# Kernel optimization log

Measured on AMD Instinct MI355X. Metric: run time of the kernel, lower is better.

The kernel has to match this reference:

```python
import jax, jax.numpy as jnp
import numpy as np
from jax import lax

SIZE = 64
N_PHASES = SIZE * (SIZE - 1) // 2  # 2016
LOSS_DB_CM = 0.5
INSERTION_LOSS_DB = LOSS_DB_CM * 0.1          # per-MZI insertion loss (dB)
LOSS_AMP = 10.0 ** (-INSERTION_LOSS_DB / 20.0)  # amplitude transmission per MZI
NONLINEAR_COEFF = 2.6e-20

# Reck triangular mesh ordering: layer i = 1..SIZE-1, MZIs on adjacent modes (j, j+1)
_MODE_IDX = np.array([j for i in range(1, SIZE) for j in range(i)], dtype=np.int32)


def build_mesh_unitary(phases):
    """Sequentially compose 2x2 MZI rotations into a SIZE x SIZE complex matrix.
    Each MZI with phase theta applies T = loss * [[cos, i sin],[i sin, cos]] to
    adjacent modes (m, m+1). U = T_K ... T_1."""
    U0 = jnp.eye(SIZE, dtype=jnp.complex64)

    def step(U, xs):
        theta, m = xs
        c = jnp.cos(theta).astype(jnp.complex64)
        s = (1j * jnp.sin(theta)).astype(jnp.complex64)
        row_a = U[m]
        row_b = U[m + 1]
        new_a = LOSS_AMP * (c * row_a + s * row_b)
        new_b = LOSS_AMP * (s * row_a + c * row_b)
        U = U.at[m].set(new_a).at[m + 1].set(new_b)
        return U, None

    U, _ = lax.scan(step, U0, (phases, jnp.asarray(_MODE_IDX)))
    return U


def setup_inputs() -> dict:
    key = jax.random.key(0)
    k1, k2, k3 = jax.random.split(key, 3)
    B = 262144
    x_real = jax.random.normal(k1, (B, SIZE), dtype=jnp.float32)
    x_imag = jax.random.normal(k2, (B, SIZE), dtype=jnp.float32)
    # nn.initializers.uniform(scale=2*pi) -> U[0, 2*pi)
    phases = jax.random.uniform(k3, (N_PHASES,), dtype=jnp.float32) * (2.0 * np.pi)
    return {"x_real": x_real, "x_imag": x_imag, "phases": phases}


def reference(x_real, x_imag, phases):
    x = (x_real + 1j * x_imag).astype(jnp.complex64)  # [B, SIZE]
    U = build_mesh_unitary(phases)                    # [SIZE, SIZE] complex64
    # vmapped mesh apply == batched matmul with the composed unitary
    out = x @ U.T                                     # [B, SIZE]
    # Kerr nonlinearity (include_nonlinearity=True)
    optical_power = jnp.abs(out) ** 2
    nonlinear_phase = NONLINEAR_COEFF * optical_power * 1000.0
    out = out * jnp.exp(1j * nonlinear_phase.astype(jnp.complex64))
    return out
```

## Files before the change

### kernel.cpp

```cpp
#include <hip/hip_runtime.h>


#define PSIZE 64
#define N_PHASES 2016
#define NLAYER 63
#define LOSS_AMP 0.99426007f
#define NL_COEFF 2.6e-17f

#define UF32_BYTES (2 * PSIZE * PSIZE * 4)
#define WSPLIT_BYTES (4 * PSIZE * PSIZE * 2)
#define WS_NEED (UF32_BYTES + WSPLIT_BYTES)

typedef __attribute__((ext_vector_type(8))) short sh8;
typedef __attribute__((ext_vector_type(4))) float f32x4;

__device__ __align__(16) float g_U_fallback[2 * PSIZE * PSIZE];

__device__ inline unsigned short f32_to_bf16_rn(float f) {
  unsigned int u = __float_as_uint(f);
  u += 0x7fffu + ((u >> 16) & 1u);
  return (unsigned short)(u >> 16);
}
__device__ inline float bf16_to_f32(unsigned short h) {
  return __uint_as_float(((unsigned int)h) << 16);
}

__device__ inline float rdlane(float v, int l) {
  return __int_as_float(__builtin_amdgcn_readlane(__float_as_int(v), l));
}

__device__ inline unsigned pkbf16(float a, float b) {
  unsigned r;
  asm("v_cvt_pk_bf16_f32 %0, %1, %2" : "=v"(r) : "v"(a), "v"(b));
  return r;
}
__device__ inline float lo16f(unsigned u) { return __uint_as_float(u << 16); }
__device__ inline float hi16f(unsigned u) {
  return __uint_as_float(u & 0xFFFF0000u);
}
__device__ inline sh8 mk8(unsigned a, unsigned b, unsigned c, unsigned d) {
  union { unsigned u[4]; sh8 s; } t;
  t.u[0] = a; t.u[1] = b; t.u[2] = c; t.u[3] = d;
  return t.s;
}

__global__ __launch_bounds__(64, 1) void build_kernel(
    const float* __restrict__ phases,
    float* __restrict__ Uf32,
    unsigned short* __restrict__ Wout) {
  const int tid = threadIdx.x;

  float wre[NLAYER], wim[NLAYER];
#pragma unroll
  for (int li = 0; li < NLAYER; ++li) {
    float c = 1.0f, s = 0.0f;
    if (tid <= li) {
      const float th = phases[(li * (li + 1)) / 2 + tid];
      c = LOSS_AMP * cosf(th);
      s = LOSS_AMP * sinf(th);
    }
    wre[li] = c;
    wim[li] = s;
  }

  float ure[PSIZE], uim[PSIZE];
#pragma unroll
  for (int r = 0; r < PSIZE; ++r) {
    ure[r] = (r == tid) ? 1.0f : 0.0f;
    uim[r] = 0.0f;
  }

#pragma unroll
  for (int li = 0; li < NLAYER; ++li) {
#pragma unroll
    for (int m = 0; m <= li; ++m) {
      const float wc = rdlane(wre[li], m);
      const float ws = rdlane(wim[li], m);
      const float are = ure[m], aim = uim[m];
      const float bre = ure[m + 1], bim = uim[m + 1];
      ure[m]     = fmaf(wc, are, -ws * bim);
      uim[m]     = fmaf(wc, aim,  ws * bre);
      ure[m + 1] = fmaf(wc, bre, -ws * aim);
      uim[m + 1] = fmaf(wc, bim,  ws * are);
    }
  }

  float* Udst = (Uf32 != nullptr) ? Uf32 : g_U_fallback;
#pragma unroll
  for (int r = 0; r < PSIZE; ++r)
    ((float2*)Udst)[r * PSIZE + tid] = make_float2(ure[r], uim[r]);

  if (Wout != nullptr) {
    const int slot = tid >> 3, kin = tid & 7;
#pragma unroll
    for (int n = 0; n < PSIZE; ++n) {
      const int base = n * 64 + ((slot ^ (n & 7)) << 3) + kin;
      const unsigned short rh = f32_to_bf16_rn(ure[n]);
      const unsigned short rl = f32_to_bf16_rn(ure[n] - bf16_to_f32(rh));
      const unsigned short ih = f32_to_bf16_rn(uim[n]);
      const unsigned short il = f32_to_bf16_rn(uim[n] - bf16_to_f32(ih));
      Wout[0 * 4096 + base] = rh;
      Wout[1 * 4096 + base] = rl;
      Wout[2 * 4096 + base] = ih;
      Wout[3 * 4096 + base] = il;
    }
  }
}

__global__ __launch_bounds__(256, 2) void apply_mfma(
    const unsigned short* __restrict__ W,
    const float* __restrict__ xr,
    const float* __restrict__ xi,
    float* __restrict__ out_re,
    float* __restrict__ out_im) {
  __shared__ __align__(16) unsigned short sW[4 * PSIZE * PSIZE];
  {
    const float4* src = (const float4*)W;
    float4* dst = (float4*)sW;
    for (int i = threadIdx.x; i < WSPLIT_BYTES / 16; i += 256) dst[i] = src[i];
  }
  __syncthreads();

  const int lane = threadIdx.x & 63;
  const int wave = threadIdx.x >> 6;
  const int lm = lane & 15;
  const int lg = lane >> 4;
  const long row0 = (long)blockIdx.x * 128 + (long)wave * 32;

  f32x4 accRe[2][4], accIm[2][4];
#pragma unroll
  for (int a = 0; a < 2; ++a)
#pragma unroll
    for (int b = 0; b < 4; ++b) {
      accRe[a][b] = f32x4{0.f, 0.f, 0.f, 0.f};
      accIm[a][b] = f32x4{0.f, 0.f, 0.f, 0.f};
    }

#pragma unroll
  for (int ks = 0; ks < 2; ++ks) {
    sh8 arh[2], arl[2], aih[2], ail[2], anh[2], anl[2];
#pragma unroll
    for (int mt = 0; mt < 2; ++mt) {
      const long r = row0 + mt * 16 + lm;
      const float4* pr = (const float4*)(xr + r * PSIZE + ks * 32 + lg * 8);
      const float4* pi = (const float4*)(xi + r * PSIZE + ks * 32 + lg * 8);
      const float4 v0 = pr[0], v1 = pr[1];
      const float4 w0 = pi[0], w1 = pi[1];

      const unsigned rh0 = pkbf16(v0.x, v0.y), rh1 = pkbf16(v0.z, v0.w);
      const unsigned rh2 = pkbf16(v1.x, v1.y), rh3 = pkbf16(v1.z, v1.w);
      const unsigned rl0 = pkbf16(v0.x - lo16f(rh0), v0.y - hi16f(rh0));
      const unsigned rl1 = pkbf16(v0.z - lo16f(rh1), v0.w - hi16f(rh1));
      const unsigned rl2 = pkbf16(v1.x - lo16f(rh2), v1.y - hi16f(rh2));
      const unsigned rl3 = pkbf16(v1.z - lo16f(rh3), v1.w - hi16f(rh3));
      arh[mt] = mk8(rh0, rh1, rh2, rh3);
      arl[mt] = mk8(rl0, rl1, rl2, rl3);

      const unsigned ih0 = pkbf16(w0.x, w0.y), ih1 = pkbf16(w0.z, w0.w);
      const unsigned ih2 = pkbf16(w1.x, w1.y), ih3 = pkbf16(w1.z, w1.w);
      const unsigned il0 = pkbf16(w0.x - lo16f(ih0), w0.y - hi16f(ih0));
      const unsigned il1 = pkbf16(w0.z - lo16f(ih1), w0.w - hi16f(ih1));
      const unsigned il2 = pkbf16(w1.x - lo16f(ih2), w1.y - hi16f(ih2));
      const unsigned il3 = pkbf16(w1.z - lo16f(ih3), w1.w - hi16f(ih3));
      aih[mt] = mk8(ih0, ih1, ih2, ih3);
      ail[mt] = mk8(il0, il1, il2, il3);
      anh[mt] = mk8(ih0 ^ 0x80008000u, ih1 ^ 0x80008000u,
                    ih2 ^ 0x80008000u, ih3 ^ 0x80008000u);
      anl[mt] = mk8(il0 ^ 0x80008000u, il1 ^ 0x80008000u,
                    il2 ^ 0x80008000u, il3 ^ 0x80008000u);
    }

#pragma unroll
    for (int nt = 0; nt < 4; ++nt) {
      const int n = nt * 16 + lm;
      const int sidx = n * 64 + (((ks * 4 + lg) ^ (n & 7)) << 3);
      const sh8 bRh = *(const sh8*)&sW[0 * 4096 + sidx];
      const sh8 bRl = *(const sh8*)&sW[1 * 4096 + sidx];
      const sh8 bIh = *(const sh8*)&sW[2 * 4096 + sidx];
      const sh8 bIl = *(const sh8*)&sW[3 * 4096 + sidx];
#pragma unroll
      for (int mt = 0; mt < 2; ++mt) {
        f32x4 cr = accRe[mt][nt];
        cr = __builtin_amdgcn_mfma_f32_16x16x32_bf16(arh[mt], bRh, cr, 0, 0, 0);
        cr = __builtin_amdgcn_mfma_f32_16x16x32_bf16(arh[mt], bRl, cr, 0, 0, 0);
        cr = __builtin_amdgcn_mfma_f32_16x16x32_bf16(arl[mt], bRh, cr, 0, 0, 0);
        cr = __builtin_amdgcn_mfma_f32_16x16x32_bf16(anh[mt], bIh, cr, 0, 0, 0);
        cr = __builtin_amdgcn_mfma_f32_16x16x32_bf16(anh[mt], bIl, cr, 0, 0, 0);
        cr = __builtin_amdgcn_mfma_f32_16x16x32_bf16(anl[mt], bIh, cr, 0, 0, 0);
        accRe[mt][nt] = cr;
        f32x4 ci = accIm[mt][nt];
        ci = __builtin_amdgcn_mfma_f32_16x16x32_bf16(arh[mt], bIh, ci, 0, 0, 0);
        ci = __builtin_amdgcn_mfma_f32_16x16x32_bf16(arh[mt], bIl, ci, 0, 0, 0);
        ci = __builtin_amdgcn_mfma_f32_16x16x32_bf16(arl[mt], bIh, ci, 0, 0, 0);
        ci = __builtin_amdgcn_mfma_f32_16x16x32_bf16(aih[mt], bRh, ci, 0, 0, 0);
        ci = __builtin_amdgcn_mfma_f32_16x16x32_bf16(aih[mt], bRl, ci, 0, 0, 0);
        ci = __builtin_amdgcn_mfma_f32_16x16x32_bf16(ail[mt], bRh, ci, 0, 0, 0);
        accIm[mt][nt] = ci;
      }
    }
  }

#pragma unroll
  for (int mt = 0; mt < 2; ++mt) {
#pragma unroll
    for (int reg = 0; reg < 4; ++reg) {
      const long row = row0 + mt * 16 + lg * 4 + reg;
#pragma unroll
      for (int nt = 0; nt < 4; ++nt) {
        const int col = nt * 16 + lm;
        const float re = accRe[mt][nt][reg];
        const float im = accIm[mt][nt][reg];
        const float p = NL_COEFF * fmaf(re, re, im * im);
        out_re[row * PSIZE + col] = fmaf(-im, p, re);
        if (out_im != nullptr) out_im[row * PSIZE + col] = fmaf(re, p, im);
      }
    }
  }
}

__global__ __launch_bounds__(256, 2) void tail_kernel(
    const float* __restrict__ Usrc,
    const float* __restrict__ xr,
    const float* __restrict__ xi,
    float* __restrict__ out_re,
    float* __restrict__ out_im,
    long rowStart, long nrows) {
  __shared__ __align__(16) float sU[2 * PSIZE * PSIZE];
  {
    const float4* g4 = (const float4*)((Usrc != nullptr) ? Usrc : g_U_fallback);
    float4* s4 = (float4*)sU;
    for (int i = threadIdx.x; i < (2 * PSIZE * PSIZE) / 4; i += 256)
      s4[i] = g4[i];
  }
  __syncthreads();

  const long row = rowStart + (long)blockIdx.x * 256 + threadIdx.x;
  if (row >= nrows) return;

  const float4* xr4 = (const float4*)(xr + (size_t)row * PSIZE);
  const float4* xi4 = (const float4*)(xi + (size_t)row * PSIZE);

  float aR[PSIZE], aI[PSIZE];
#pragma unroll
  for (int j = 0; j < PSIZE; ++j) { aR[j] = 0.0f; aI[j] = 0.0f; }

  const float4* su4 = (const float4*)sU;

#pragma unroll 1
  for (int kc = 0; kc < 8; ++kc) {
    const float4 a0 = xr4[2 * kc];
    const float4 a1 = xr4[2 * kc + 1];
    const float4 b0 = xi4[2 * kc];
    const float4 b1 = xi4[2 * kc + 1];
    const float4* up = su4 + kc * 4;
#pragma unroll
    for (int j = 0; j < PSIZE; ++j) {
      const float4 u0 = up[j * 32 + 0];
      const float4 u1 = up[j * 32 + 1];
      const float4 u2 = up[j * 32 + 2];
      const float4 u3 = up[j * 32 + 3];
      float r = aR[j], m = aI[j];
      r = fmaf(a0.x, u0.x, r); r = fmaf(-b0.x, u0.y, r);
      m = fmaf(a0.x, u0.y, m); m = fmaf( b0.x, u0.x, m);
      r = fmaf(a0.y, u0.z, r); r = fmaf(-b0.y, u0.w, r);
      m = fmaf(a0.y, u0.w, m); m = fmaf( b0.y, u0.z, m);
      r = fmaf(a0.z, u1.x, r); r = fmaf(-b0.z, u1.y, r);
      m = fmaf(a0.z, u1.y, m); m = fmaf( b0.z, u1.x, m);
      r = fmaf(a0.w, u1.z, r); r = fmaf(-b0.w, u1.w, r);
      m = fmaf(a0.w, u1.w, m); m = fmaf( b0.w, u1.z, m);
      r = fmaf(a1.x, u2.x, r); r = fmaf(-b1.x, u2.y, r);
      m = fmaf(a1.x, u2.y, m); m = fmaf( b1.x, u2.x, m);
      r = fmaf(a1.y, u2.z, r); r = fmaf(-b1.y, u2.w, r);
      m = fmaf(a1.y, u2.w, m); m = fmaf( b1.y, u2.z, m);
      r = fmaf(a1.z, u3.x, r); r = fmaf(-b1.z, u3.y, r);
      m = fmaf(a1.z, u3.y, m); m = fmaf( b1.z, u3.x, m);
      r = fmaf(a1.w, u3.z, r); r = fmaf(-b1.w, u3.w, r);
      m = fmaf(a1.w, u3.w, m); m = fmaf( b1.w, u3.z, m);
      aR[j] = r; aI[j] = m;
    }
  }

  float* orp = out_re + (size_t)row * PSIZE;
  float* oip = (out_im != nullptr) ? (out_im + (size_t)row * PSIZE) : nullptr;
#pragma unroll
  for (int jq = 0; jq < 16; ++jq) {
    const int j = 4 * jq;
    float4 vr, vi;
    {
      const float p = NL_COEFF * fmaf(aR[j], aR[j], aI[j] * aI[j]);
      vr.x = fmaf(-aI[j], p, aR[j]); vi.x = fmaf(aR[j], p, aI[j]);
    }
    {
      const float p = NL_COEFF * fmaf(aR[j+1], aR[j+1], aI[j+1] * aI[j+1]);
      vr.y = fmaf(-aI[j+1], p, aR[j+1]); vi.y = fmaf(aR[j+1], p, aI[j+1]);
    }
    {
      const float p = NL_COEFF * fmaf(aR[j+2], aR[j+2], aI[j+2] * aI[j+2]);
      vr.z = fmaf(-aI[j+2], p, aR[j+2]); vi.z = fmaf(aR[j+2], p, aI[j+2]);
    }
    {
      const float p = NL_COEFF * fmaf(aR[j+3], aR[j+3], aI[j+3] * aI[j+3]);
      vr.w = fmaf(-aI[j+3], p, aR[j+3]); vi.w = fmaf(aR[j+3], p, aI[j+3]);
    }
    ((float4*)orp)[jq] = vr;
    if (oip != nullptr) ((float4*)oip)[jq] = vi;
  }
}

extern "C" void kernel_launch(void* const* d_in, const int* in_sizes, int n_in,
                              void* d_out, int out_size, void* d_ws, size_t ws_size,
                              hipStream_t stream) {
  int pidx = -1;
  for (int i = 0; i < n_in; ++i) {
    if (in_sizes[i] == N_PHASES) { pidx = i; break; }
  }
  if (pidx < 0) pidx = 2;
  int xa = -1, xb = -1;
  for (int i = 0; i < n_in; ++i) {
    if (i == pidx) continue;
    if (xa < 0) xa = i;
    else if (xb < 0) xb = i;
  }
  if (xa < 0 || xb < 0) return;

  const float* phases = (const float*)d_in[pidx];
  const float* x_real = (const float*)d_in[xa];
  const float* x_imag = (const float*)d_in[xb];

  long b_in = (long)in_sizes[xa] / PSIZE;
  if ((long)in_sizes[xb] / PSIZE < b_in) b_in = (long)in_sizes[xb] / PSIZE;

  float* out = (float*)d_out;
  float* out_re = out;
  float* out_im = nullptr;
  long nrows;

  if ((long)out_size >= 2 * b_in * PSIZE) {
    const long half = (long)out_size / 2;
    out_im = out + half;
    long cap = half / PSIZE;
    nrows = (b_in < cap) ? b_in : cap;
  } else {
    long cap = (long)out_size / PSIZE;
    nrows = (b_in < cap) ? b_in : cap;
  }
  if (nrows <= 0) return;

  float* Uf32 = nullptr;
  unsigned short* Wsplit = nullptr;
  if (d_ws != nullptr && ws_size >= (size_t)WS_NEED) {
    Uf32 = (float*)d_ws;
    Wsplit = (unsigned short*)((char*)d_ws + UF32_BYTES);
  }

  build_kernel<<<1, 64, 0, stream>>>(phases, Uf32, Wsplit);

  const long ntiles = (Wsplit != nullptr) ? (nrows / 128) : 0;
  if (ntiles > 0) {
    apply_mfma<<<(int)ntiles, 256, 0, stream>>>(Wsplit, x_real, x_imag,
                                                out_re, out_im);
  }
  const long done = ntiles * 128;
  if (done < nrows) {
    const long rem = nrows - done;
    const int tblocks = (int)((rem + 255) / 256);
    tail_kernel<<<tblocks, 256, 0, stream>>>(Uf32, x_real, x_imag,
                                             out_re, out_im, done, nrows);
  }
}
```

Measured before the change: 276.2 us.

## Parallelize mesh unitary build across waves via layer-chunk products

The single-wave sequential composition of 63 MZI layers is split so four waves each compose 16 layers into a partial unitary. The partials are then combined with complex 64x64 matmuls in shared memory by all eight waves. This shortens the serial critical path of the build kernel, which runs on one block ahead of the batched apply. It adds shared-memory traffic and extra matmul flops, and changes the floating-point rounding order.

New measurement: 231.7 us. -16.1%, faster.

```diff
diff --git a/kernel.cpp b/kernel.cpp
--- a/kernel.cpp
+++ b/kernel.cpp
@@ -44,61 +44,115 @@
   return t.s;
 }
 
-__global__ __launch_bounds__(64, 1) void build_kernel(
+__global__ __launch_bounds__(512, 1) void build_kernel(
     const float* __restrict__ phases,
     float* __restrict__ Uf32,
     unsigned short* __restrict__ Wout) {
+  __shared__ float2 sS[3][PSIZE * PSIZE];
+  __shared__ float2 sWsm[PSIZE * PSIZE];
   const int tid = threadIdx.x;
-
-  float wre[NLAYER], wim[NLAYER];
-#pragma unroll
-  for (int li = 0; li < NLAYER; ++li) {
-    float c = 1.0f, s = 0.0f;
-    if (tid <= li) {
-      const float th = phases[(li * (li + 1)) / 2 + tid];
-      c = LOSS_AMP * cosf(th);
-      s = LOSS_AMP * sinf(th);
-    }
-    wre[li] = c;
-    wim[li] = s;
-  }
+  const int wv = tid >> 6;
+  const int lane = tid & 63;
+
+  for (int idx = tid; idx < PSIZE * PSIZE; idx += 512) {
+    const int li = idx >> 6;
+    const int m = idx & 63;
+    float2 w = make_float2(1.0f, 0.0f);
+    if (li < NLAYER && m <= li) {
+      const float th = phases[(li * (li + 1)) / 2 + m];
+      w = make_float2(LOSS_AMP * cosf(th), LOSS_AMP * sinf(th));
+    }
+    sWsm[idx] = w;
+  }
+  __syncthreads();
 
   float ure[PSIZE], uim[PSIZE];
-#pragma unroll
-  for (int r = 0; r < PSIZE; ++r) {
-    ure[r] = (r == tid) ? 1.0f : 0.0f;
-    uim[r] = 0.0f;
-  }
-
-#pragma unroll
-  for (int li = 0; li < NLAYER; ++li) {
-#pragma unroll
-    for (int m = 0; m <= li; ++m) {
-      const float wc = rdlane(wre[li], m);
-      const float ws = rdlane(wim[li], m);
-      const float are = ure[m], aim = uim[m];
-      const float bre = ure[m + 1], bim = uim[m + 1];
-      ure[m]     = fmaf(wc, are, -ws * bim);
-      uim[m]     = fmaf(wc, aim,  ws * bre);
-      ure[m + 1] = fmaf(wc, bre, -ws * aim);
-      uim[m + 1] = fmaf(wc, bim,  ws * are);
+  if (wv < 4) {
+#pragma unroll
+    for (int r = 0; r < PSIZE; ++r) {
+      ure[r] = (r == lane) ? 1.0f : 0.0f;
+      uim[r] = 0.0f;
+    }
+    for (int l = 0; l < 16; ++l) {
+      const int li = wv * 16 + l;
+      const float2 w2 = sWsm[li * 64 + lane];
+#pragma unroll
+      for (int m = 0; m < NLAYER; ++m) {
+        const float wc = rdlane(w2.x, m);
+        const float ws = rdlane(w2.y, m);
+        const float are = ure[m], aim = uim[m];
+        const float bre = ure[m + 1], bim = uim[m + 1];
+        ure[m]     = fmaf(wc, are, -ws * bim);
+        uim[m]     = fmaf(wc, aim,  ws * bre);
+        ure[m + 1] = fmaf(wc, bre, -ws * aim);
+        uim[m + 1] = fmaf(wc, bim,  ws * are);
+      }
+    }
+  }
+  __syncthreads();
+
+  if (wv < 4) {
+    float2* dst = (wv == 3) ? sWsm : sS[wv];
+#pragma unroll
+    for (int r = 0; r < PSIZE; ++r)
+      dst[r * 64 + lane] = make_float2(ure[r], uim[r]);
+  }
+  __syncthreads();
+
+  const int wg = wv >> 2;
+  const int w4 = wv & 3;
+  {
+    const float2* A  = (wg == 0) ? sS[1] : sWsm;
+    const float2* Bm = (wg == 0) ? sS[0] : sS[2];
+    float pre[16], pim[16];
+#pragma unroll
+    for (int r = 0; r < 16; ++r) { pre[r] = 0.f; pim[r] = 0.f; }
+    for (int m = 0; m < PSIZE; ++m) {
+      const float2 b = Bm[m * 64 + lane];
+#pragma unroll
+      for (int r = 0; r < 16; ++r) {
+        const float2 a = A[(16 * w4 + r) * 64 + m];
+        pre[r] = fmaf(a.x, b.x, fmaf(-a.y, b.y, pre[r]));
+        pim[r] = fmaf(a.x, b.y, fmaf( a.y, b.x, pim[r]));
+      }
+    }
+    __syncthreads();
+    float2* Pd = (wg == 0) ? sS[0] : sS[1];
+#pragma unroll
+    for (int r = 0; r < 16; ++r)
+      Pd[(16 * w4 + r) * 64 + lane] = make_float2(pre[r], pim[r]);
+  }
+  __syncthreads();
+
+  float fre[8], fim[8];
+#pragma unroll
+  for (int r = 0; r < 8; ++r) { fre[r] = 0.f; fim[r] = 0.f; }
+  for (int m = 0; m < PSIZE; ++m) {
+    const float2 b = sS[0][m * 64 + lane];
+#pragma unroll
+    for (int r = 0; r < 8; ++r) {
+      const float2 a = sS[1][(8 * wv + r) * 64 + m];
+      fre[r] = fmaf(a.x, b.x, fmaf(-a.y, b.y, fre[r]));
+      fim[r] = fmaf(a.x, b.y, fmaf( a.y, b.x, fim[r]));
     }
   }
 
   float* Udst = (Uf32 != nullptr) ? Uf32 : g_U_fallback;
 #pragma unroll
-  for (int r = 0; r < PSIZE; ++r)
-    ((float2*)Udst)[r * PSIZE + tid] = make_float2(ure[r], uim[r]);
-
+  for (int r = 0; r < 8; ++r) {
+    const int rr = 8 * wv + r;
+    ((float2*)Udst)[rr * 64 + lane] = make_float2(fre[r], fim[r]);
+  }
   if (Wout != nullptr) {
-    const int slot = tid >> 3, kin = tid & 7;
-#pragma unroll
-    for (int n = 0; n < PSIZE; ++n) {
+    const int slot = lane >> 3, kin = lane & 7;
+#pragma unroll
+    for (int r = 0; r < 8; ++r) {
+      const int n = 8 * wv + r;
       const int base = n * 64 + ((slot ^ (n & 7)) << 3) + kin;
-      const unsigned short rh = f32_to_bf16_rn(ure[n]);
-      const unsigned short rl = f32_to_bf16_rn(ure[n] - bf16_to_f32(rh));
-      const unsigned short ih = f32_to_bf16_rn(uim[n]);
-      const unsigned short il = f32_to_bf16_rn(uim[n] - bf16_to_f32(ih));
+      const unsigned short rh = f32_to_bf16_rn(fre[r]);
+      const unsigned short rl = f32_to_bf16_rn(fre[r] - bf16_to_f32(rh));
+      const unsigned short ih = f32_to_bf16_rn(fim[r]);
+      const unsigned short il = f32_to_bf16_rn(fim[r] - bf16_to_f32(ih));
       Wout[0 * 4096 + base] = rh;
       Wout[1 * 4096 + base] = rl;
       Wout[2 * 4096 + base] = ih;
@@ -353,7 +407,7 @@
     Wsplit = (unsigned short*)((char*)d_ws + UF32_BYTES);
   }
 
-  build_kernel<<<1, 64, 0, stream>>>(phases, Uf32, Wsplit);
+  build_kernel<<<1, 512, 0, stream>>>(phases, Uf32, Wsplit);
 
   const long ntiles = (Wsplit != nullptr) ? (nrows / 128) : 0;
   if (ntiles > 0) {
```
